# Kernel tuning notes

Hardware: AMD Instinct MI355X
Metric: run time of the kernel (lower is better)

The kernel has to match this reference:

```python
import jax, jax.numpy as jnp
import numpy as np

N, E = 50000, 800000
IN, HID, LAT = 512, 256, 128


def setup_inputs() -> dict:
    key = jax.random.key(0)
    ks = jax.random.split(key, 9)
    x = jax.random.normal(ks[0], (N, IN), dtype=jnp.float32)
    edge_index = jax.random.randint(ks[1], (2, E), 0, N, dtype=jnp.int64)
    edge_attr = jax.random.uniform(ks[2], (E,), dtype=jnp.float32)
    # GCNConv weights (glorot-ish scaling) and biases
    W1 = jax.random.normal(ks[3], (IN, HID), dtype=jnp.float32) / np.sqrt(IN)
    b1 = jnp.zeros((HID,), dtype=jnp.float32)
    W_mu = jax.random.normal(ks[4], (HID, LAT), dtype=jnp.float32) / np.sqrt(HID)
    b_mu = jnp.zeros((LAT,), dtype=jnp.float32)
    W_lv = jax.random.normal(ks[5], (HID, LAT), dtype=jnp.float32) / np.sqrt(HID)
    b_lv = jnp.zeros((LAT,), dtype=jnp.float32)
    return {"x": x, "edge_index": edge_index, "edge_attr": edge_attr,
            "W1": W1, "b1": b1, "W_mu": W_mu, "b_mu": b_mu,
            "W_lv": W_lv, "b_lv": b_lv}


def _gcn_norm(edge_index, edge_attr, num_nodes):
    # GCNConv default: add self-loops (weight 1), symmetric normalization
    loops = jnp.arange(num_nodes, dtype=edge_index.dtype)
    src = jnp.concatenate([edge_index[0], loops])
    dst = jnp.concatenate([edge_index[1], loops])
    w = jnp.concatenate([edge_attr, jnp.ones((num_nodes,), edge_attr.dtype)])
    deg = jax.ops.segment_sum(w, dst, num_segments=num_nodes)
    dis = jnp.where(deg > 0, jax.lax.rsqrt(jnp.maximum(deg, 1e-12)), 0.0)
    norm = dis[src] * w * dis[dst]  # [E + N]
    return src, dst, norm


def reference(x, edge_index, edge_attr, W1, b1, W_mu, b_mu, W_lv, b_lv):
    num_nodes = x.shape[0]
    src, dst, norm = _gcn_norm(edge_index, edge_attr, num_nodes)

    def conv(h, W, b):
        m = h @ W                      # dense transform [N, out]
        msg = m[src] * norm[:, None]   # gather + scale  [E+N, out]
        return jax.ops.segment_sum(msg, dst, num_segments=num_nodes) + b

    hidden = jax.nn.relu(conv(x, W1, b1))
    # Dropout(0.2) is identity in eval mode
    mu = conv(hidden, W_mu, b_mu)
    logvar = conv(hidden, W_lv, b_lv)
    return (mu, logvar)
```

## Files before the change

### kernel.cpp

```cpp
#include <hip/hip_runtime.h>

#define IN_F 512
#define HID_F 256
#define LAT_F 128

typedef __bf16 bf16x8 __attribute__((ext_vector_type(8)));
typedef float floatx4 __attribute__((ext_vector_type(4)));

#define FIX_SCALE 1048576.0f

__device__ __forceinline__ unsigned short f2bf(float f) {
    union { float f; unsigned u; } v; v.f = f;
    unsigned r = (v.u + 0x7fff + ((v.u >> 16) & 1)) >> 16;
    return (unsigned short)r;
}
__device__ __forceinline__ float bf2f(unsigned short h) {
    union { unsigned u; float f; } v; v.u = ((unsigned)h) << 16;
    return v.f;
}

__device__ __forceinline__ void gload_lds16(const void* g, void* lds) {
    __builtin_amdgcn_global_load_lds(
        (const __attribute__((address_space(1))) unsigned int*)(uintptr_t)g,
        (__attribute__((address_space(3))) unsigned int*)(uintptr_t)lds,
        16, 0, 0);
}


__global__ void prep_all(const float* __restrict__ W1, const float* __restrict__ Wmu,
                         const float* __restrict__ Wlv, unsigned long long* __restrict__ packed,
                         unsigned short* __restrict__ W1t, unsigned short* __restrict__ B2t,
                         int N) {
    int t = blockIdx.x * 256 + threadIdx.x;
    if (t < N) packed[t] = (1ULL << 32) | (unsigned long long)(unsigned)FIX_SCALE;
    if (t < HID_F * IN_F) {
        int n = t >> 9, k = t & 511;
        W1t[t] = f2bf(W1[(size_t)k * HID_F + n]);
    }
    if (t < HID_F * HID_F) {
        int n = t >> 8, k = t & 255;
        float v = (n < 128) ? Wmu[(size_t)k * LAT_F + n] : Wlv[(size_t)k * LAT_F + (n - 128)];
        B2t[t] = f2bf(v);
    }
}


__global__ void edge_deg(const int* __restrict__ ei, const float* __restrict__ attr,
                         unsigned long long* __restrict__ packed, int* __restrict__ slot, int E) {
    int e = blockIdx.x * 256 + threadIdx.x;
    if (e < E) {
        int d = ei[E + e];
        unsigned fw = __float2uint_rn(attr[e] * FIX_SCALE);
        unsigned long long old = atomicAdd(&packed[d], (1ULL << 32) | (unsigned long long)fw);
        slot[e] = (int)(old >> 32);
    }
}


__global__ void scan_blocks(const unsigned long long* __restrict__ packed,
                            float* __restrict__ dis, int* __restrict__ excl,
                            int* __restrict__ blockSums, int N) {
    __shared__ int sdata[256];
    int tid = threadIdx.x;
    int base = blockIdx.x * 1024 + tid * 4;
    int v[4]; int sum = 0;
#pragma unroll
    for (int j = 0; j < 4; ++j) {
        int c = 0;
        if (base + j < N) {
            unsigned long long p = packed[base + j];
            c = (int)(p >> 32);
            float dg = (float)(unsigned)(p & 0xffffffffu) * (1.0f / FIX_SCALE);
            dis[base + j] = dg > 0.f ? rsqrtf(fmaxf(dg, 1e-12f)) : 0.f;
        }
        v[j] = c; sum += c;
    }
    sdata[tid] = sum;
    __syncthreads();
    for (int off = 1; off < 256; off <<= 1) {
        int t = (tid >= off) ? sdata[tid - off] : 0;
        __syncthreads();
        sdata[tid] += t;
        __syncthreads();
    }
    if (tid == 255) blockSums[blockIdx.x] = sdata[255];
    int run = sdata[tid] - sum;
#pragma unroll
    for (int j = 0; j < 4; ++j) { if (base + j < N) excl[base + j] = run; run += v[j]; }
}

__global__ void scan_sums(int* blockSums, int NB) {
    __shared__ int s[64];
    int tid = threadIdx.x;
    int v = (tid < NB) ? blockSums[tid] : 0;
    s[tid] = v;
    __syncthreads();
    for (int off = 1; off < 64; off <<= 1) {
        int t = (tid >= off) ? s[tid - off] : 0;
        __syncthreads();
        s[tid] += t;
        __syncthreads();
    }
    if (tid < NB) blockSums[tid] = s[tid] - v;
}

__global__ void scan_add(int* row_ptr, const int* __restrict__ blockSums, int N, int total) {
    int tid = threadIdx.x;
    int base = blockIdx.x * 1024 + tid * 4;
    int add = blockSums[blockIdx.x];
#pragma unroll
    for (int j = 0; j < 4; ++j) if (base + j < N) row_ptr[base + j] += add;
    if (blockIdx.x == 0 && tid == 0) row_ptr[N] = total;
}


__global__ void fill_csr(const int* __restrict__ ei, const float* __restrict__ attr,
                         const int* __restrict__ slot, const float* __restrict__ dis,
                         const int* __restrict__ row_ptr,
                         int* __restrict__ col, float* __restrict__ val, int E, int N) {
    int e = blockIdx.x * 256 + threadIdx.x;
    if (e >= E + N) return;
    int s, d, sl; float w;
    if (e < E) { s = ei[e]; d = ei[E + e]; w = attr[e]; sl = slot[e]; }
    else       { s = d = e - E; w = 1.0f; sl = 0; }
    int pos = row_ptr[d] + sl;
    col[pos] = s;
    val[pos] = dis[s] * w * dis[d];
}


template <bool ABF16>
__global__ __launch_bounds__(256) void gemm_mfma(const void* __restrict__ Avoid,
                                                 const unsigned short* __restrict__ Bt,
                                                 unsigned short* __restrict__ C,
                                                 int M, int K) {
    __shared__ unsigned short As[2][64 * 32];
    __shared__ unsigned short Bs[2][256 * 32];
    int tid = threadIdx.x;
    int wave = tid >> 6, lane = tid & 63;
    int mrow = lane & 15, quad = lane >> 4;
    int blockRow = blockIdx.x * 64;

    const unsigned short* Abf = (const unsigned short*)Avoid;
    const float*          Afp = (const float*)Avoid;

    floatx4 acc[4][4];
#pragma unroll
    for (int i = 0; i < 4; ++i)
#pragma unroll
        for (int j = 0; j < 4; ++j) acc[i][j] = (floatx4){0.f, 0.f, 0.f, 0.f};

    int r = tid >> 2;
    int kq = tid & 3;
    int arow = blockRow + r; if (arow >= M) arow = M - 1;

    if constexpr (ABF16) {
        gload_lds16(Abf + (size_t)arow * K + kq * 8, &As[0][wave * 512]);
    } else {
        const float* p = Afp + (size_t)arow * K + kq * 8;
        float4 a0 = *(const float4*)p, a1 = *(const float4*)(p + 4);
        unsigned short h[8] = {f2bf(a0.x), f2bf(a0.y), f2bf(a0.z), f2bf(a0.w),
                               f2bf(a1.x), f2bf(a1.y), f2bf(a1.z), f2bf(a1.w)};
        *(uint4*)&As[0][r * 32 + kq * 8] = *(uint4*)h;
    }
#pragma unroll
    for (int pass = 0; pass < 4; ++pass)
        gload_lds16(Bt + (size_t)(r + pass * 64) * K + kq * 8,
                    &Bs[0][(pass * 256 + wave * 64) * 8]);

    int cur = 0;
    for (int k0 = 0; k0 < K; k0 += 32) {
        __syncthreads();
        int kn = k0 + 32;
        bool more = kn < K;
        float4 a0, a1;
        if (more) {
            if constexpr (ABF16) {
                gload_lds16(Abf + (size_t)arow * K + kn + kq * 8, &As[cur ^ 1][wave * 512]);
            } else {
                const float* p = Afp + (size_t)arow * K + kn + kq * 8;
                a0 = *(const float4*)p; a1 = *(const float4*)(p + 4);
            }
#pragma unroll
            for (int pass = 0; pass < 4; ++pass)
                gload_lds16(Bt + (size_t)(r + pass * 64) * K + kn + kq * 8,
                            &Bs[cur ^ 1][(pass * 256 + wave * 64) * 8]);
        }
        bf16x8 af[4];
#pragma unroll
        for (int i = 0; i < 4; ++i)
            af[i] = *(const bf16x8*)&As[cur][(i * 16 + mrow) * 32 + quad * 8];
#pragma unroll
        for (int j = 0; j < 4; ++j) {
            bf16x8 bf = *(const bf16x8*)&Bs[cur][(wave * 64 + j * 16 + mrow) * 32 + quad * 8];
#pragma unroll
            for (int i = 0; i < 4; ++i)
                acc[i][j] = __builtin_amdgcn_mfma_f32_16x16x32_bf16(af[i], bf, acc[i][j], 0, 0, 0);
        }
        if (!ABF16 && more) {
            unsigned short h[8] = {f2bf(a0.x), f2bf(a0.y), f2bf(a0.z), f2bf(a0.w),
                                   f2bf(a1.x), f2bf(a1.y), f2bf(a1.z), f2bf(a1.w)};
            *(uint4*)&As[cur ^ 1][r * 32 + kq * 8] = *(uint4*)h;
        }
        cur ^= 1;
    }
#pragma unroll
    for (int i = 0; i < 4; ++i)
#pragma unroll
        for (int j = 0; j < 4; ++j) {
            int colo = wave * 64 + j * 16 + mrow;
#pragma unroll
            for (int v = 0; v < 4; ++v) {
                int row = blockRow + i * 16 + quad * 4 + v;
                if (row < M) C[(size_t)row * HID_F + colo] = f2bf(acc[i][j][v]);
            }
        }
}


__global__ void agg_relu(const unsigned short* __restrict__ m, const int* __restrict__ row_ptr,
                         const int* __restrict__ col, const float* __restrict__ val,
                         const float* __restrict__ bias, unsigned short* __restrict__ hidden) {
    int i = blockIdx.x, l = threadIdx.x, c0 = l << 2;
    int p0 = __builtin_amdgcn_readfirstlane(row_ptr[i]);
    int p1 = __builtin_amdgcn_readfirstlane(row_ptr[i + 1]);
    float a0 = 0.f, a1 = 0.f, a2 = 0.f, a3 = 0.f;
    for (int p = p0; p < p1; p += 8) {
        int sj[8]; float wj[8];
#pragma unroll
        for (int j = 0; j < 8; ++j) {
            int q = p + j;
            bool ok = q < p1; if (!ok) q = p1 - 1;
            sj[j] = col[q];
            wj[j] = ok ? val[q] : 0.f;
        }
        ushort4 u[8];
#pragma unroll
        for (int j = 0; j < 8; ++j)
            u[j] = *(const ushort4*)(m + (size_t)sj[j] * HID_F + c0);
#pragma unroll
        for (int j = 0; j < 8; ++j) {
            a0 = fmaf(bf2f(u[j].x), wj[j], a0);
            a1 = fmaf(bf2f(u[j].y), wj[j], a1);
            a2 = fmaf(bf2f(u[j].z), wj[j], a2);
            a3 = fmaf(bf2f(u[j].w), wj[j], a3);
        }
    }
    float4 b = *(const float4*)(bias + c0);
    a0 = fmaxf(a0 + b.x, 0.f); a1 = fmaxf(a1 + b.y, 0.f);
    a2 = fmaxf(a2 + b.z, 0.f); a3 = fmaxf(a3 + b.w, 0.f);
    ushort4 o = make_ushort4(f2bf(a0), f2bf(a1), f2bf(a2), f2bf(a3));
    *(ushort4*)(hidden + (size_t)i * HID_F + c0) = o;
}

__global__ void agg_out(const unsigned short* __restrict__ m, const int* __restrict__ row_ptr,
                        const int* __restrict__ col, const float* __restrict__ val,
                        const float* __restrict__ bmu, const float* __restrict__ blv,
                        float* __restrict__ out, int N) {
    int i = blockIdx.x, l = threadIdx.x, c0 = l << 2;
    int p0 = __builtin_amdgcn_readfirstlane(row_ptr[i]);
    int p1 = __builtin_amdgcn_readfirstlane(row_ptr[i + 1]);
    float a0 = 0.f, a1 = 0.f, a2 = 0.f, a3 = 0.f;
    for (int p = p0; p < p1; p += 8) {
        int sj[8]; float wj[8];
#pragma unroll
        for (int j = 0; j < 8; ++j) {
            int q = p + j;
            bool ok = q < p1; if (!ok) q = p1 - 1;
            sj[j] = col[q];
            wj[j] = ok ? val[q] : 0.f;
        }
        ushort4 u[8];
#pragma unroll
        for (int j = 0; j < 8; ++j)
            u[j] = *(const ushort4*)(m + (size_t)sj[j] * HID_F + c0);
#pragma unroll
        for (int j = 0; j < 8; ++j) {
            a0 = fmaf(bf2f(u[j].x), wj[j], a0);
            a1 = fmaf(bf2f(u[j].y), wj[j], a1);
            a2 = fmaf(bf2f(u[j].z), wj[j], a2);
            a3 = fmaf(bf2f(u[j].w), wj[j], a3);
        }
    }
    if (l < 32) {
        float4 b = *(const float4*)(bmu + c0);
        float4 o = make_float4(a0 + b.x, a1 + b.y, a2 + b.z, a3 + b.w);
        *(float4*)(out + (size_t)i * LAT_F + c0) = o;
    } else {
        int c = c0 - 128;
        float4 b = *(const float4*)(blv + c);
        float4 o = make_float4(a0 + b.x, a1 + b.y, a2 + b.z, a3 + b.w);
        *(float4*)(out + (size_t)(N + i) * LAT_F + c) = o;
    }
}


extern "C" void kernel_launch(void* const* d_in, const int* in_sizes, int n_in,
                              void* d_out, int out_size, void* d_ws, size_t ws_size,
                              hipStream_t stream) {
    const float* x    = (const float*)d_in[0];
    const int*   ei   = (const int*)d_in[1];
    const float* attr = (const float*)d_in[2];
    const float* W1   = (const float*)d_in[3];
    const float* b1   = (const float*)d_in[4];
    const float* Wmu  = (const float*)d_in[5];
    const float* bmu  = (const float*)d_in[6];
    const float* Wlv  = (const float*)d_in[7];
    const float* blv  = (const float*)d_in[8];
    float* out = (float*)d_out;

    const int N  = in_sizes[0] / IN_F;
    const int E  = in_sizes[2];
    const int EN = E + N;

    char* w = (char*)d_ws;
    size_t off = 0;
    auto carve = [&](size_t bytes) -> void* {
        void* p = w + off; off += (bytes + 255) & ~(size_t)255; return p;
    };
    unsigned long long* packed = (unsigned long long*)carve((size_t)N * 8);
    float*          dis       = (float*)carve((size_t)N * 4);
    int*            row_ptr   = (int*)  carve((size_t)(N + 1) * 4);
    int*            blockSums = (int*)  carve(64 * 4);
    int*            slot      = (int*)  carve((size_t)E * 4);
    int*            col       = (int*)  carve((size_t)EN * 4);
    float*          val       = (float*)carve((size_t)EN * 4);
    unsigned short* W1t       = (unsigned short*)carve((size_t)HID_F * IN_F * 2);
    unsigned short* B2t       = (unsigned short*)carve((size_t)HID_F * HID_F * 2);
    unsigned short* m         = (unsigned short*)carve((size_t)N * HID_F * 2);
    unsigned short* hidden    = (unsigned short*)carve((size_t)N * HID_F * 2);

    prep_all<<<(HID_F * IN_F + 255) / 256, 256, 0, stream>>>(W1, Wmu, Wlv, packed, W1t, B2t, N);

    edge_deg<<<(E + 255) / 256, 256, 0, stream>>>(ei, attr, packed, slot, E);

    int NB = (N + 1023) / 1024;
    scan_blocks<<<NB, 256, 0, stream>>>(packed, dis, row_ptr, blockSums, N);
    scan_sums<<<1, 64, 0, stream>>>(blockSums, NB);
    scan_add<<<NB, 256, 0, stream>>>(row_ptr, blockSums, N, EN);

    fill_csr<<<(EN + 255) / 256, 256, 0, stream>>>(ei, attr, slot, dis, row_ptr, col, val, E, N);

    int gblocks = (N + 63) / 64;
    gemm_mfma<false><<<gblocks, 256, 0, stream>>>(x, W1t, m, N, IN_F);
    agg_relu<<<N, 64, 0, stream>>>(m, row_ptr, col, val, b1, hidden);
    gemm_mfma<true><<<gblocks, 256, 0, stream>>>(hidden, B2t, m, N, HID_F);
    agg_out<<<N, 64, 0, stream>>>(m, row_ptr, col, val, bmu, blv, out, N);
}
```

Before: 419.0 us.

## Keep GEMM weight fragments in registers with persistent blocks and swizzled LDS A tiles

Replaces the per-block GEMM, which streamed both A and B through LDS, with a persistent 256-block, 512-thread kernel. Each wave loads its slice of the weight matrix once into registers, in an MFMA-fragment layout pre-arranged by prep_all, and reuses it across all row tiles. A is staged through an XOR-swizzled, double-buffered LDS tile in 128-wide K chunks, and the next chunk is prefetched into registers. The aim is to cut repeated B loads from global memory and LDS and to reduce bank conflicts, at the cost of heavy register pressure (up to 32 bf16x8 fragments per lane for K=512), which may limit occupancy.

```diff
diff --git a/kernel.cpp b/kernel.cpp
--- a/kernel.cpp
+++ b/kernel.cpp
@@ -19,28 +19,25 @@
     return v.f;
 }
 
-__device__ __forceinline__ void gload_lds16(const void* g, void* lds) {
-    __builtin_amdgcn_global_load_lds(
-        (const __attribute__((address_space(1))) unsigned int*)(uintptr_t)g,
-        (__attribute__((address_space(3))) unsigned int*)(uintptr_t)lds,
-        16, 0, 0);
-}
-
 
 __global__ void prep_all(const float* __restrict__ W1, const float* __restrict__ Wmu,
                          const float* __restrict__ Wlv, unsigned long long* __restrict__ packed,
-                         unsigned short* __restrict__ W1t, unsigned short* __restrict__ B2t,
+                         unsigned short* __restrict__ Bf1, unsigned short* __restrict__ Bf2,
                          int N) {
     int t = blockIdx.x * 256 + threadIdx.x;
     if (t < N) packed[t] = (1ULL << 32) | (unsigned long long)(unsigned)FIX_SCALE;
     if (t < HID_F * IN_F) {
-        int n = t >> 9, k = t & 511;
-        W1t[t] = f2bf(W1[(size_t)k * HID_F + n]);
+        int j = t & 7, l = (t >> 3) & 63, jj = (t >> 9) & 1, ks = (t >> 10) & 15, w = t >> 14;
+        int n = w * 32 + jj * 16 + (l & 15);
+        int k = ks * 32 + (l >> 4) * 8 + j;
+        Bf1[t] = f2bf(W1[(size_t)k * HID_F + n]);
     }
     if (t < HID_F * HID_F) {
-        int n = t >> 8, k = t & 255;
+        int j = t & 7, l = (t >> 3) & 63, jj = (t >> 9) & 1, ks = (t >> 10) & 7, w = t >> 13;
+        int n = w * 32 + jj * 16 + (l & 15);
+        int k = ks * 32 + (l >> 4) * 8 + j;
         float v = (n < 128) ? Wmu[(size_t)k * LAT_F + n] : Wlv[(size_t)k * LAT_F + (n - 128)];
-        B2t[t] = f2bf(v);
+        Bf2[t] = f2bf(v);
     }
 }
 
@@ -129,92 +126,112 @@
 }
 
 
-template <bool ABF16>
-__global__ __launch_bounds__(256) void gemm_mfma(const void* __restrict__ Avoid,
-                                                 const unsigned short* __restrict__ Bt,
-                                                 unsigned short* __restrict__ C,
-                                                 int M, int K) {
-    __shared__ unsigned short As[2][64 * 32];
-    __shared__ unsigned short Bs[2][256 * 32];
+template <bool ABF16, int KK>
+__global__ __launch_bounds__(512, 2) void gemm_breg(const void* __restrict__ Avoid,
+                                                    const unsigned short* __restrict__ Bfrag,
+                                                    unsigned short* __restrict__ C,
+                                                    int M, int ntiles) {
+    constexpr int NKS = KK / 32;
+    constexpr int S   = KK / 128;
+    __shared__ unsigned short As[2][64 * 128];
+
     int tid = threadIdx.x;
     int wave = tid >> 6, lane = tid & 63;
     int mrow = lane & 15, quad = lane >> 4;
-    int blockRow = blockIdx.x * 64;
 
     const unsigned short* Abf = (const unsigned short*)Avoid;
     const float*          Afp = (const float*)Avoid;
 
-    floatx4 acc[4][4];
+    bf16x8 bfr[NKS][2];
+#pragma unroll
+    for (int ks = 0; ks < NKS; ++ks)
+#pragma unroll
+        for (int jj = 0; jj < 2; ++jj)
+            bfr[ks][jj] = *(const bf16x8*)(Bfrag +
+                ((((size_t)wave * NKS + ks) * 2 + jj) * 64 + lane) * 8);
+
+    int c  = tid & 15;
+    int r0 = tid >> 4;
+    int cs0 = (c ^ (r0 & 7)) << 3;
+    int cs1 = (c ^ ((r0 + 32) & 7)) << 3;
+
+    float4 a0, a1, a2, a3;
+    uint4  u0, u1;
+
+    auto issue = [&](int t_, int s_) {
+        int g0 = t_ * 64 + r0;       if (g0 >= M) g0 = M - 1;
+        int g1 = t_ * 64 + r0 + 32;  if (g1 >= M) g1 = M - 1;
+        if constexpr (ABF16) {
+            u0 = *(const uint4*)(Abf + (size_t)g0 * KK + s_ * 128 + c * 8);
+            u1 = *(const uint4*)(Abf + (size_t)g1 * KK + s_ * 128 + c * 8);
+        } else {
+            const float* p0 = Afp + (size_t)g0 * KK + s_ * 128 + c * 8;
+            const float* p1 = Afp + (size_t)g1 * KK + s_ * 128 + c * 8;
+            a0 = *(const float4*)p0; a1 = *(const float4*)(p0 + 4);
+            a2 = *(const float4*)p1; a3 = *(const float4*)(p1 + 4);
+        }
+    };
+
+    floatx4 acc[4][2];
 #pragma unroll
     for (int i = 0; i < 4; ++i)
 #pragma unroll
-        for (int j = 0; j < 4; ++j) acc[i][j] = (floatx4){0.f, 0.f, 0.f, 0.f};
-
-    int r = tid >> 2;
-    int kq = tid & 3;
-    int arow = blockRow + r; if (arow >= M) arow = M - 1;
-
-    if constexpr (ABF16) {
-        gload_lds16(Abf + (size_t)arow * K + kq * 8, &As[0][wave * 512]);
-    } else {
-        const float* p = Afp + (size_t)arow * K + kq * 8;
-        float4 a0 = *(const float4*)p, a1 = *(const float4*)(p + 4);
-        unsigned short h[8] = {f2bf(a0.x), f2bf(a0.y), f2bf(a0.z), f2bf(a0.w),
-                               f2bf(a1.x), f2bf(a1.y), f2bf(a1.z), f2bf(a1.w)};
-        *(uint4*)&As[0][r * 32 + kq * 8] = *(uint4*)h;
-    }
-#pragma unroll
-    for (int pass = 0; pass < 4; ++pass)
-        gload_lds16(Bt + (size_t)(r + pass * 64) * K + kq * 8,
-                    &Bs[0][(pass * 256 + wave * 64) * 8]);
-
+        for (int jj = 0; jj < 2; ++jj) acc[i][jj] = (floatx4){0.f, 0.f, 0.f, 0.f};
+
+    int tile = blockIdx.x;
+    if (tile < ntiles) issue(tile, 0);
     int cur = 0;
-    for (int k0 = 0; k0 < K; k0 += 32) {
-        __syncthreads();
-        int kn = k0 + 32;
-        bool more = kn < K;
-        float4 a0, a1;
-        if (more) {
+
+    for (; tile < ntiles; tile += gridDim.x) {
+#pragma unroll
+        for (int s = 0; s < S; ++s) {
             if constexpr (ABF16) {
-                gload_lds16(Abf + (size_t)arow * K + kn + kq * 8, &As[cur ^ 1][wave * 512]);
+                *(uint4*)&As[cur][r0 * 128 + cs0] = u0;
+                *(uint4*)&As[cur][(r0 + 32) * 128 + cs1] = u1;
             } else {
-                const float* p = Afp + (size_t)arow * K + kn + kq * 8;
-                a0 = *(const float4*)p; a1 = *(const float4*)(p + 4);
+                unsigned short h0[8] = {f2bf(a0.x), f2bf(a0.y), f2bf(a0.z), f2bf(a0.w),
+                                        f2bf(a1.x), f2bf(a1.y), f2bf(a1.z), f2bf(a1.w)};
+                unsigned short h1[8] = {f2bf(a2.x), f2bf(a2.y), f2bf(a2.z), f2bf(a2.w),
+                                        f2bf(a3.x), f2bf(a3.y), f2bf(a3.z), f2bf(a3.w)};
+                *(uint4*)&As[cur][r0 * 128 + cs0] = *(uint4*)h0;
+                *(uint4*)&As[cur][(r0 + 32) * 128 + cs1] = *(uint4*)h1;
             }
-#pragma unroll
-            for (int pass = 0; pass < 4; ++pass)
-                gload_lds16(Bt + (size_t)(r + pass * 64) * K + kn + kq * 8,
-                            &Bs[cur ^ 1][(pass * 256 + wave * 64) * 8]);
-        }
-        bf16x8 af[4];
+            if (s + 1 < S) issue(tile, s + 1);
+            else if (tile + (int)gridDim.x < ntiles) issue(tile + gridDim.x, 0);
+
+            asm volatile("s_waitcnt lgkmcnt(0)" ::: "memory");
+            __builtin_amdgcn_s_barrier();
+
+#pragma unroll
+            for (int ks = 0; ks < 4; ++ks) {
+#pragma unroll
+                for (int i = 0; i < 4; ++i) {
+                    int row = i * 16 + mrow;
+                    bf16x8 af = *(const bf16x8*)&As[cur][row * 128 +
+                                    (((ks * 4 + quad) ^ (row & 7)) << 3)];
+#pragma unroll
+                    for (int jj = 0; jj < 2; ++jj)
+                        acc[i][jj] = __builtin_amdgcn_mfma_f32_16x16x32_bf16(
+                            af, bfr[s * 4 + ks][jj], acc[i][jj], 0, 0, 0);
+                }
+            }
+            asm volatile("s_waitcnt lgkmcnt(0)" ::: "memory");
+            __builtin_amdgcn_s_barrier();
+            cur ^= 1;
+        }
 #pragma unroll
         for (int i = 0; i < 4; ++i)
-            af[i] = *(const bf16x8*)&As[cur][(i * 16 + mrow) * 32 + quad * 8];
-#pragma unroll
-        for (int j = 0; j < 4; ++j) {
-            bf16x8 bf = *(const bf16x8*)&Bs[cur][(wave * 64 + j * 16 + mrow) * 32 + quad * 8];
-#pragma unroll
-            for (int i = 0; i < 4; ++i)
-                acc[i][j] = __builtin_amdgcn_mfma_f32_16x16x32_bf16(af[i], bf, acc[i][j], 0, 0, 0);
-        }
-        if (!ABF16 && more) {
-            unsigned short h[8] = {f2bf(a0.x), f2bf(a0.y), f2bf(a0.z), f2bf(a0.w),
-                                   f2bf(a1.x), f2bf(a1.y), f2bf(a1.z), f2bf(a1.w)};
-            *(uint4*)&As[cur ^ 1][r * 32 + kq * 8] = *(uint4*)h;
-        }
-        cur ^= 1;
-    }
-#pragma unroll
-    for (int i = 0; i < 4; ++i)
-#pragma unroll
-        for (int j = 0; j < 4; ++j) {
-            int colo = wave * 64 + j * 16 + mrow;
-#pragma unroll
-            for (int v = 0; v < 4; ++v) {
-                int row = blockRow + i * 16 + quad * 4 + v;
-                if (row < M) C[(size_t)row * HID_F + colo] = f2bf(acc[i][j][v]);
+#pragma unroll
+            for (int jj = 0; jj < 2; ++jj) {
+                int colo = wave * 32 + jj * 16 + mrow;
+#pragma unroll
+                for (int v = 0; v < 4; ++v) {
+                    int row = tile * 64 + i * 16 + quad * 4 + v;
+                    if (row < M) C[(size_t)row * HID_F + colo] = f2bf(acc[i][jj][v]);
+                }
+                acc[i][jj] = (floatx4){0.f, 0.f, 0.f, 0.f};
             }
-        }
+    }
 }
 
 
@@ -325,12 +342,12 @@
     int*            slot      = (int*)  carve((size_t)E * 4);
     int*            col       = (int*)  carve((size_t)EN * 4);
     float*          val       = (float*)carve((size_t)EN * 4);
-    unsigned short* W1t       = (unsigned short*)carve((size_t)HID_F * IN_F * 2);
-    unsigned short* B2t       = (unsigned short*)carve((size_t)HID_F * HID_F * 2);
+    unsigned short* Bf1       = (unsigned short*)carve((size_t)HID_F * IN_F * 2);
+    unsigned short* Bf2       = (unsigned short*)carve((size_t)HID_F * HID_F * 2);
     unsigned short* m         = (unsigned short*)carve((size_t)N * HID_F * 2);
     unsigned short* hidden    = (unsigned short*)carve((size_t)N * HID_F * 2);
 
-    prep_all<<<(HID_F * IN_F + 255) / 256, 256, 0, stream>>>(W1, Wmu, Wlv, packed, W1t, B2t, N);
+    prep_all<<<(HID_F * IN_F + 255) / 256, 256, 0, stream>>>(W1, Wmu, Wlv, packed, Bf1, Bf2, N);
 
     edge_deg<<<(E + 255) / 256, 256, 0, stream>>>(ei, attr, packed, slot, E);
 
@@ -341,9 +358,9 @@
 
     fill_csr<<<(EN + 255) / 256, 256, 0, stream>>>(ei, attr, slot, dis, row_ptr, col, val, E, N);
 
-    int gblocks = (N + 63) / 64;
-    gemm_mfma<false><<<gblocks, 256, 0, stream>>>(x, W1t, m, N, IN_F);
+    int ntiles = (N + 63) / 64;
+    gemm_breg<false, IN_F><<<256, 512, 0, stream>>>(x, Bf1, m, N, ntiles);
     agg_relu<<<N, 64, 0, stream>>>(m, row_ptr, col, val, b1, hidden);
-    gemm_mfma<true><<<gblocks, 256, 0, stream>>>(hidden, B2t, m, N, HID_F);
+    gemm_breg<true, HID_F><<<256, 512, 0, stream>>>(hidden, Bf2, m, N, ntiles);
     agg_out<<<N, 64, 0, stream>>>(m, row_ptr, col, val, bmu, blv, out, N);
 }
```

After: 403.2 us. 1.04x faster.
